# Optimization experiments

Hardware: AMD Instinct MI355X
Metric: run time of the kernel (lower is better)

The kernel has to match this reference:

```python
import jax, jax.numpy as jnp
import numpy as np

D_MODEL = 2048
R = 32
LN_EPS = 1e-5  # torch nn.LayerNorm default


def setup_inputs() -> dict:
    key = jax.random.key(0)
    k_x, k_wd, k_wu = jax.random.split(key, 3)
    x = jax.random.normal(k_x, (4, 4096, D_MODEL), dtype=jnp.float32)
    gamma = jnp.ones((D_MODEL,), dtype=jnp.float32)
    beta = jnp.zeros((D_MODEL,), dtype=jnp.float32)
    # down: default torch Linear init ~ U(-1/sqrt(d), 1/sqrt(d)); approximate with scaled normal
    w_down = jax.random.normal(k_wd, (D_MODEL, R), dtype=jnp.float32) / jnp.sqrt(jnp.float32(D_MODEL))
    b_down = jnp.zeros((R,), dtype=jnp.float32)
    # up: nn.init.normal_(std=0.001), bias zero
    w_up = jax.random.normal(k_wu, (R, D_MODEL), dtype=jnp.float32) * 0.001
    b_up = jnp.zeros((D_MODEL,), dtype=jnp.float32)
    return {"x": x, "gamma": gamma, "beta": beta, "w_down": w_down,
            "b_down": b_down, "w_up": w_up, "b_up": b_up}


def reference(x, gamma, beta, w_down, b_down, w_up, b_up):
    # LayerNorm over last dim
    mu = jnp.mean(x, axis=-1, keepdims=True)
    var = jnp.mean(jnp.square(x - mu), axis=-1, keepdims=True)
    h = (x - mu) * jax.lax.rsqrt(var + LN_EPS) * gamma + beta
    # down-proj -> exact GELU (torch nn.GELU default) -> up-proj -> residual
    h = jnp.einsum('bsd,dr->bsr', h, w_down) + b_down
    h = jax.nn.gelu(h, approximate=False)
    h = jnp.einsum('bsr,rd->bsd', h, w_up) + b_up
    return x + h
```

## Files before the change

### kernel.cpp

```cpp
#include <hip/hip_runtime.h>
#include <math.h>

#define D     2048
#define NR    32
#define ROWS  8

typedef short bf16x8 __attribute__((ext_vector_type(8)));
typedef float f32x4  __attribute__((ext_vector_type(4)));

__device__ __forceinline__ unsigned int f2bf(float f) {
    unsigned int u = __float_as_uint(f);
    return (u + 0x7FFFu + ((u >> 16) & 1u)) >> 16;
}
__device__ __forceinline__ unsigned int pk2(float a, float b) {
    return f2bf(a) | (f2bf(b) << 16);
}

__global__ __launch_bounds__(64)
void k_prep(const float* __restrict__ wd, const float* __restrict__ gamma,
            const float* __restrict__ beta, const float* __restrict__ wu,
            unsigned int* __restrict__ wuf, unsigned int* __restrict__ wdpf,
            float* __restrict__ c12p)
{
    const int l = threadIdx.x;
    const int q = l >> 4, p = l & 15;
    const int b = blockIdx.x;
    if (b < 128) {
        const int t = b;
        float v[8];
        #pragma unroll
        for (int e = 0; e < 8; ++e)
            v[e] = wu[(q * 8 + e) * D + t * 16 + p];
        uint4 pk;
        pk.x = pk2(v[0], v[1]); pk.y = pk2(v[2], v[3]);
        pk.z = pk2(v[4], v[5]); pk.w = pk2(v[6], v[7]);
        *(uint4*)&wuf[(t * 64 + l) * 4] = pk;
    } else {
        const int idx = b - 128;
        const int kk = idx >> 1, n = idx & 1;
        const int r = n * 16 + p;
        float wv[8];
        float c1 = 0.f, c2 = 0.f;
        #pragma unroll
        for (int e = 0; e < 8; ++e) {
            const int k = kk * 32 + q * 8 + e;
            const float wdv = wd[k * NR + r];
            wv[e] = gamma[k] * wdv;
            c1 += wv[e];
            c2 += beta[k] * wdv;
        }
        uint4 pk;
        pk.x = pk2(wv[0], wv[1]); pk.y = pk2(wv[2], wv[3]);
        pk.z = pk2(wv[4], wv[5]); pk.w = pk2(wv[6], wv[7]);
        *(uint4*)&wdpf[(idx * 64 + l) * 4] = pk;
        c1 += __shfl_xor(c1, 16); c1 += __shfl_xor(c1, 32);
        c2 += __shfl_xor(c2, 16); c2 += __shfl_xor(c2, 32);
        if (q == 0) {
            c12p[idx * 32 + p]      = c1;
            c12p[idx * 32 + 16 + p] = c2;
        }
    }
}

__global__ __launch_bounds__(64)
void k_c12(const float* __restrict__ c12p, float* __restrict__ c12)
{
    const int i = threadIdx.x;
    const int half = i >> 5, r = i & 31;
    const int n = r >> 4, rr = r & 15;
    float s = 0.f;
    for (int kk = 0; kk < 64; ++kk)
        s += c12p[(kk * 2 + n) * 32 + half * 16 + rr];
    c12[i] = s;
}

__global__ __launch_bounds__(256, 4)
void k_fused(const float* __restrict__ x, const float* __restrict__ bd,
             const float* __restrict__ bu, const unsigned int* __restrict__ wuf,
             const unsigned int* __restrict__ wdpf, const float* __restrict__ c12,
             float* __restrict__ out)
{
    __shared__ unsigned int xs[ROWS * 1024];
    __shared__ float Sp[4][2][16][8];
    __shared__ unsigned short a_sh[ROWS][NR];
    __shared__ float mu_s[ROWS], rs_s[ROWS];

    const int tid = threadIdx.x;
    const int w = tid >> 6, l = tid & 63;
    const int p = l & 15, q = l >> 4;
    const long row0 = (long)blockIdx.x * ROWS;

    #pragma unroll
    for (int rp = 0; rp < 2; ++rp) {
        const int row = w * 2 + rp;
        const float* xr = x + (row0 + row) * D;
        float s = 0.f, s2 = 0.f;
        #pragma unroll
        for (int it = 0; it < 8; ++it) {
            const int j = it * 256 + l * 4;
            float4 v = *(const float4*)(xr + j);
            uint2 pkk;
            pkk.x = pk2(v.x, v.y);
            pkk.y = pk2(v.z, v.w);
            const int byte = (row * 4096 + j * 2) ^ (row << 4);
            *(uint2*)((char*)xs + byte) = pkk;
            s  += v.x + v.y + v.z + v.w;
            s2 += v.x * v.x + v.y * v.y + v.z * v.z + v.w * v.w;
        }
        #pragma unroll
        for (int off = 32; off >= 1; off >>= 1) {
            s  += __shfl_xor(s, off);
            s2 += __shfl_xor(s2, off);
        }
        if (l == 0) {
            const float mu  = s * (1.0f / D);
            const float var = s2 * (1.0f / D) - mu * mu;
            mu_s[row] = mu;
            rs_s[row] = rsqrtf(var + 1e-5f);
        }
    }
    __syncthreads();

    {
        f32x4 acc0 = {0.f, 0.f, 0.f, 0.f}, acc1 = {0.f, 0.f, 0.f, 0.f};
        const bool arow = p < ROWS;
        #pragma unroll 4
        for (int t = 0; t < 16; ++t) {
            bf16x8 af = {0, 0, 0, 0, 0, 0, 0, 0};
            if (arow) {
                const int byte = (p * 4096 + (w * 512 + t * 32) * 2 + q * 16) ^ (p << 4);
                af = *(const bf16x8*)((const char*)xs + byte);
            }
            const int base = (w * 16 + t) * 512 + l * 4;
            const bf16x8 b0 = *(const bf16x8*)&wdpf[base];
            const bf16x8 b1 = *(const bf16x8*)&wdpf[base + 256];
            acc0 = __builtin_amdgcn_mfma_f32_16x16x32_bf16(af, b0, acc0, 0, 0, 0);
            acc1 = __builtin_amdgcn_mfma_f32_16x16x32_bf16(af, b1, acc1, 0, 0, 0);
        }
        if (l < 32) {
            *(f32x4*)&Sp[w][0][p][(q & 1) * 4] = acc0;
            *(f32x4*)&Sp[w][1][p][(q & 1) * 4] = acc1;
        }
    }
    __syncthreads();

    {
        const int m = tid >> 5, r = tid & 31;
        const int n = r >> 4, rr = r & 15;
        const float S = Sp[0][n][rr][m] + Sp[1][n][rr][m]
                      + Sp[2][n][rr][m] + Sp[3][n][rr][m];
        const float y = rs_s[m] * (S - mu_s[m] * c12[r]) + c12[32 + r] + bd[r];
        const float a = 0.5f * y * (1.0f + erff(y * 0.70710678118654752f));
        a_sh[m][r] = (unsigned short)f2bf(a);
    }
    __syncthreads();

    {
        bf16x8 afc = {0, 0, 0, 0, 0, 0, 0, 0};
        if (p < ROWS) afc = *(const bf16x8*)((const char*)a_sh + p * 64 + q * 16);
        const bool act = p < ROWS;
        const long xbase = (row0 + p) * D;
        const f32x4 z = {0.f, 0.f, 0.f, 0.f};
        #pragma unroll 4
        for (int t = 0; t < 32; ++t) {
            const int j0 = w * 512 + t * 16;
            const bf16x8 bw = *(const bf16x8*)&wuf[(j0 >> 4) * 256 + l * 4];
            f32x4 dd = __builtin_amdgcn_mfma_f32_16x16x32_bf16(bw, afc, z, 0, 0, 0);
            if (act) {
                const int jj = j0 + q * 4;
                const float4 xv = *(const float4*)(x + xbase + jj);
                const float4 bv = *(const float4*)(bu + jj);
                float* op = out + xbase + jj;
                __builtin_nontemporal_store(xv.x + bv.x + dd[0], op + 0);
                __builtin_nontemporal_store(xv.y + bv.y + dd[1], op + 1);
                __builtin_nontemporal_store(xv.z + bv.z + dd[2], op + 2);
                __builtin_nontemporal_store(xv.w + bv.w + dd[3], op + 3);
            }
        }
    }
}

extern "C" void kernel_launch(void* const* d_in, const int* in_sizes, int n_in,
                              void* d_out, int out_size, void* d_ws, size_t ws_size,
                              hipStream_t stream) {
    (void)n_in; (void)ws_size; (void)out_size;
    const float* x     = (const float*)d_in[0];
    const float* gamma = (const float*)d_in[1];
    const float* beta  = (const float*)d_in[2];
    const float* wd    = (const float*)d_in[3];
    const float* bd    = (const float*)d_in[4];
    const float* wu    = (const float*)d_in[5];
    const float* bu    = (const float*)d_in[6];
    float* out = (float*)d_out;

    unsigned int* wuf  = (unsigned int*)d_ws;
    unsigned int* wdpf = wuf + 32768;
    float* c12p = (float*)(wdpf + 32768);
    float* c12  = c12p + 4096;

    const int nrows  = in_sizes[0] / D;
    const int blocks = nrows / ROWS;

    hipLaunchKernelGGL(k_prep,  dim3(256),    dim3(64),  0, stream,
                       wd, gamma, beta, wu, wuf, wdpf, c12p);
    hipLaunchKernelGGL(k_c12,   dim3(1),      dim3(64),  0, stream, c12p, c12);
    hipLaunchKernelGGL(k_fused, dim3(blocks), dim3(256), 0, stream,
                       x, bd, bu, wuf, wdpf, c12, out);
}
```

Measured before the change: 287.5 us.

## Process 16 rows per block with 512 threads to fill MFMA tiles

Doubles rows per block to 16 and threads to 512 (8 waves), so the 16-row MFMA A operand is fully used instead of half zero-padded. Waves are split into 4 K-slices by 2 output-column halves for the down-projection, and each wave in the up-projection covers 256 columns. Output stores become a single vector nontemporal store. It also halves the block count and doubles LDS per block (about 64KB of x staging), which may lower occupancy.

After: 274.3 us. 4.6% less time.

```diff
diff --git a/kernel.cpp b/kernel.cpp
--- a/kernel.cpp
+++ b/kernel.cpp
@@ -3,7 +3,7 @@
 
 #define D     2048
 #define NR    32
-#define ROWS  8
+#define ROWS  16
 
 typedef short bf16x8 __attribute__((ext_vector_type(8)));
 typedef float f32x4  __attribute__((ext_vector_type(4)));
@@ -74,14 +74,14 @@
     c12[i] = s;
 }
 
-__global__ __launch_bounds__(256, 4)
+__global__ __launch_bounds__(512, 4)
 void k_fused(const float* __restrict__ x, const float* __restrict__ bd,
              const float* __restrict__ bu, const unsigned int* __restrict__ wuf,
              const unsigned int* __restrict__ wdpf, const float* __restrict__ c12,
              float* __restrict__ out)
 {
     __shared__ unsigned int xs[ROWS * 1024];
-    __shared__ float Sp[4][2][16][8];
+    __shared__ float Sp[8][16][16];
     __shared__ unsigned short a_sh[ROWS][NR];
     __shared__ float mu_s[ROWS], rs_s[ROWS];
 
@@ -122,33 +122,25 @@
     __syncthreads();
 
     {
-        f32x4 acc0 = {0.f, 0.f, 0.f, 0.f}, acc1 = {0.f, 0.f, 0.f, 0.f};
-        const bool arow = p < ROWS;
+        const int ks = w & 3, n = w >> 2;
+        f32x4 acc = {0.f, 0.f, 0.f, 0.f};
         #pragma unroll 4
         for (int t = 0; t < 16; ++t) {
-            bf16x8 af = {0, 0, 0, 0, 0, 0, 0, 0};
-            if (arow) {
-                const int byte = (p * 4096 + (w * 512 + t * 32) * 2 + q * 16) ^ (p << 4);
-                af = *(const bf16x8*)((const char*)xs + byte);
-            }
-            const int base = (w * 16 + t) * 512 + l * 4;
-            const bf16x8 b0 = *(const bf16x8*)&wdpf[base];
-            const bf16x8 b1 = *(const bf16x8*)&wdpf[base + 256];
-            acc0 = __builtin_amdgcn_mfma_f32_16x16x32_bf16(af, b0, acc0, 0, 0, 0);
-            acc1 = __builtin_amdgcn_mfma_f32_16x16x32_bf16(af, b1, acc1, 0, 0, 0);
+            const int byte = (p * 4096 + (ks * 512 + t * 32) * 2 + q * 16) ^ (p << 4);
+            const bf16x8 af = *(const bf16x8*)((const char*)xs + byte);
+            const int kk = ks * 16 + t;
+            const bf16x8 bf = *(const bf16x8*)&wdpf[(kk * 2 + n) * 256 + l * 4];
+            acc = __builtin_amdgcn_mfma_f32_16x16x32_bf16(af, bf, acc, 0, 0, 0);
         }
-        if (l < 32) {
-            *(f32x4*)&Sp[w][0][p][(q & 1) * 4] = acc0;
-            *(f32x4*)&Sp[w][1][p][(q & 1) * 4] = acc1;
-        }
+        *(f32x4*)&Sp[w][p][q * 4] = acc;
     }
     __syncthreads();
 
     {
         const int m = tid >> 5, r = tid & 31;
         const int n = r >> 4, rr = r & 15;
-        const float S = Sp[0][n][rr][m] + Sp[1][n][rr][m]
-                      + Sp[2][n][rr][m] + Sp[3][n][rr][m];
+        const float S = Sp[4 * n + 0][rr][m] + Sp[4 * n + 1][rr][m]
+                      + Sp[4 * n + 2][rr][m] + Sp[4 * n + 3][rr][m];
         const float y = rs_s[m] * (S - mu_s[m] * c12[r]) + c12[32 + r] + bd[r];
         const float a = 0.5f * y * (1.0f + erff(y * 0.70710678118654752f));
         a_sh[m][r] = (unsigned short)f2bf(a);
@@ -156,26 +148,23 @@
     __syncthreads();
 
     {
-        bf16x8 afc = {0, 0, 0, 0, 0, 0, 0, 0};
-        if (p < ROWS) afc = *(const bf16x8*)((const char*)a_sh + p * 64 + q * 16);
-        const bool act = p < ROWS;
+        const bf16x8 afc = *(const bf16x8*)((const char*)a_sh + p * 64 + q * 16);
         const long xbase = (row0 + p) * D;
         const f32x4 z = {0.f, 0.f, 0.f, 0.f};
         #pragma unroll 4
-        for (int t = 0; t < 32; ++t) {
-            const int j0 = w * 512 + t * 16;
-            const bf16x8 bw = *(const bf16x8*)&wuf[(j0 >> 4) * 256 + l * 4];
+        for (int t = 0; t < 16; ++t) {
+            const int j0 = w * 256 + t * 16;
+            const bf16x8 bw = *(const bf16x8*)&wuf[(w * 16 + t) * 256 + l * 4];
             f32x4 dd = __builtin_amdgcn_mfma_f32_16x16x32_bf16(bw, afc, z, 0, 0, 0);
-            if (act) {
-                const int jj = j0 + q * 4;
-                const float4 xv = *(const float4*)(x + xbase + jj);
-                const float4 bv = *(const float4*)(bu + jj);
-                float* op = out + xbase + jj;
-                __builtin_nontemporal_store(xv.x + bv.x + dd[0], op + 0);
-                __builtin_nontemporal_store(xv.y + bv.y + dd[1], op + 1);
-                __builtin_nontemporal_store(xv.z + bv.z + dd[2], op + 2);
-                __builtin_nontemporal_store(xv.w + bv.w + dd[3], op + 3);
-            }
+            const int jj = j0 + q * 4;
+            const float4 xv = *(const float4*)(x + xbase + jj);
+            const float4 bv = *(const float4*)(bu + jj);
+            f32x4 o;
+            o[0] = xv.x + bv.x + dd[0];
+            o[1] = xv.y + bv.y + dd[1];
+            o[2] = xv.z + bv.z + dd[2];
+            o[3] = xv.w + bv.w + dd[3];
+            __builtin_nontemporal_store(o, (f32x4*)(out + xbase + jj));
         }
     }
 }
@@ -204,6 +193,6 @@
     hipLaunchKernelGGL(k_prep,  dim3(256),    dim3(64),  0, stream,
                        wd, gamma, beta, wu, wuf, wdpf, c12p);
     hipLaunchKernelGGL(k_c12,   dim3(1),      dim3(64),  0, stream, c12p, c12);
-    hipLaunchKernelGGL(k_fused, dim3(blocks), dim3(256), 0, stream,
+    hipLaunchKernelGGL(k_fused, dim3(blocks), dim3(512), 0, stream,
                        x, bd, bu, wuf, wdpf, c12, out);
 }
```
